# Kernel optimization log

Hardware: AMD Instinct MI355X
Metric: run time of the kernel (lower is better)

## Reference

```python
import jax, jax.numpy as jnp
import numpy as np

NUM_HEADS = 12
HEAD_DIM = 64
LOGIT_SCALE_MAX = 4.605170185988092  # log(1/0.01), open_clip default
EPS = 1e-12  # F.normalize eps


def setup_inputs() -> dict:
    key = jax.random.key(0)
    ks = jax.random.split(key, 8)
    N, L, C = 2, 2048, 768
    return {
        "x": jax.random.normal(ks[0], (N, L, C), dtype=jnp.float32),
        "in_proj_w": jax.random.normal(ks[1], (3 * C, C), dtype=jnp.float32) * 0.02,
        "in_proj_b": jax.random.normal(ks[2], (3 * C,), dtype=jnp.float32) * 0.02,
        "logit_scale": jax.random.normal(ks[3], (NUM_HEADS, 1, 1), dtype=jnp.float32),
        "learned_scale": jnp.ones((NUM_HEADS,), dtype=jnp.float32),
        "out_proj_w": jax.random.normal(ks[4], (C, C), dtype=jnp.float32) * 0.02,
        "out_proj_b": jax.random.normal(ks[5], (C,), dtype=jnp.float32) * 0.02,
        "attn_mask": jnp.zeros((L, L), dtype=jnp.float32),
    }


def _l2norm(t):
    # F.normalize(dim=-1): x / max(||x||, eps)
    n = jnp.linalg.norm(t, axis=-1, keepdims=True)
    return t / jnp.maximum(n, EPS)


def reference(x, in_proj_w, in_proj_b, logit_scale, learned_scale,
              out_proj_w, out_proj_b, attn_mask):
    N, L, C = x.shape
    H, D = NUM_HEADS, HEAD_DIM
    # packed QKV projection: [N, L, 3C]
    qkv = jnp.einsum("nlc,fc->nlf", x, in_proj_w) + in_proj_b
    q, k, v = jnp.split(qkv, 3, axis=-1)
    # [N, L, C] -> [N, H, L, D]
    to_heads = lambda t: t.reshape(N, L, H, D).transpose(0, 2, 1, 3)
    q, k, v = to_heads(q), to_heads(k), to_heads(v)
    # cosine attention with clamped exp logit scale per head
    attn = jnp.einsum("nhld,nhmd->nhlm", _l2norm(q), _l2norm(k))
    ls = jnp.exp(jnp.minimum(logit_scale, LOGIT_SCALE_MAX))  # [H,1,1]
    attn = attn * ls[None]  # broadcast over [N,H,L,L]
    attn = attn + attn_mask  # additive mask [L,L]
    attn = jax.nn.softmax(attn, axis=-1)
    out = jnp.einsum("nhlm,nhmd->nhld", attn, v)
    # learned per-head output scale
    out = out * learned_scale[None, :, None, None]
    # [N,H,L,D] -> [N,L,C]
    out = out.transpose(0, 2, 1, 3).reshape(N, L, C)
    out = jnp.einsum("nlc,fc->nlf", out, out_proj_w) + out_proj_b
    return out
```

## Files before the change

### kernel.cpp

```cpp
#include <hip/hip_runtime.h>
#include <math.h>

#define NB   2
#define SEQ  2048
#define CH   768
#define NH   12
#define HD   64
#define F3   2304
#define LSMAX 4.605170185988092f
#define LOG2E 1.4426950408889634f
#define RESCALE_THR 8.0f
#define EXP2F(x) __builtin_amdgcn_exp2f(x)

typedef _Float16 f16;
typedef __attribute__((ext_vector_type(8))) _Float16 f16x8;
typedef __attribute__((ext_vector_type(4))) _Float16 f16x4;
typedef __attribute__((ext_vector_type(2))) _Float16 f16x2;
typedef __attribute__((ext_vector_type(4))) float f32x4;
typedef __attribute__((ext_vector_type(16))) float f32x16;

typedef __attribute__((address_space(3))) void lds_void;
typedef __attribute__((address_space(1))) const void gbl_cvoid;

#define QSZ   3145728
#define OATT  (3 * QSZ)
#define XHOFF 12582912
#define W1OFF 15728640
#define W2OFF 17498112
#define FLAGO 18087936

#define VCH   2048
#define VPLN  131072

#define GP2  72

#define KOFF(s, b) (((s) * 2 + (b)) * 2048)
#define VOFF(s, b) (8192 + ((s) * 2 + (b)) * 2304)

__global__ __launch_bounds__(256) void cvt_f16(const float* __restrict__ X,
                                               const float* __restrict__ W1,
                                               const float* __restrict__ W2,
                                               const float* __restrict__ M,
                                               f16* __restrict__ Xh,
                                               f16* __restrict__ W1h,
                                               f16* __restrict__ W2h,
                                               int* __restrict__ flag)
{
    int tid = blockIdx.x * 256 + threadIdx.x;
    if (blockIdx.y == 3) {
        if (tid < 1048576) {
            float4 v = ((const float4*)M)[tid];
            bool nz = (v.x != 0.f) || (v.y != 0.f) || (v.z != 0.f) || (v.w != 0.f);
            if (__any(nz) && (threadIdx.x & 63) == 0) atomicOr(flag, 1);
        }
        return;
    }
    const float* src; f16* dst; int n4;
    switch (blockIdx.y) {
        case 0:  src = X;  dst = Xh;  n4 = 786432;  break;
        case 1:  src = W1; dst = W1h; n4 = 442368;  break;
        default: src = W2; dst = W2h; n4 = 147456;  break;
    }
    if (tid < n4) {
        float4 v = ((const float4*)src)[tid];
        f16x4 o = {(f16)v.x, (f16)v.y, (f16)v.z, (f16)v.w};
        ((f16x4*)dst)[tid] = o;
    }
}

__global__ __launch_bounds__(256, 4) void qkv_gemm(const f16* __restrict__ Xh,
                                                   const f16* __restrict__ Wh,
                                                   const float* __restrict__ bias,
                                                   const float* __restrict__ logit_scale,
                                                   f16* __restrict__ qkv16)
{
    __shared__ f16 As[2][128 * 32];
    __shared__ f16 Bs[2][128 * 32];
    const int t    = threadIdx.x;
    const int w    = t >> 6;
    const int lane = t & 63;
    const int quad = lane >> 4;
    const int sub  = lane & 15;
    const int wm   = w & 1, wn = w >> 1;
    const int f0   = blockIdx.x * 128;
    const int m0   = blockIdx.y * 128;

    const int s0 = t, s1 = 256 + t;
    const int r0 = s0 >> 2, cb0 = ((s0 & 3) ^ (r0 & 3)) * 8;
    const int r1 = s1 >> 2, cb1 = ((s1 & 3) ^ (r1 & 3)) * 8;
    const f16* ga0 = Xh + (size_t)(m0 + r0) * CH + cb0;
    const f16* ga1 = Xh + (size_t)(m0 + r1) * CH + cb1;
    const f16* gb0 = Wh + (size_t)(f0 + r0) * CH + cb0;
    const f16* gb1 = Wh + (size_t)(f0 + r1) * CH + cb1;

    f32x4 acc[4][4];
#pragma unroll
    for (int i = 0; i < 4; ++i)
#pragma unroll
        for (int j = 0; j < 4; ++j) acc[i][j] = (f32x4){0.f, 0.f, 0.f, 0.f};

    const int pch = (quad ^ (sub & 3)) * 8;

    __builtin_amdgcn_global_load_lds((gbl_cvoid*)(ga0), (lds_void*)&As[0][s0 * 8], 16, 0, 0);
    __builtin_amdgcn_global_load_lds((gbl_cvoid*)(ga1), (lds_void*)&As[0][s1 * 8], 16, 0, 0);
    __builtin_amdgcn_global_load_lds((gbl_cvoid*)(gb0), (lds_void*)&Bs[0][s0 * 8], 16, 0, 0);
    __builtin_amdgcn_global_load_lds((gbl_cvoid*)(gb1), (lds_void*)&Bs[0][s1 * 8], 16, 0, 0);
    __syncthreads();

    for (int k0 = 0; k0 < CH; k0 += 32) {
        const int cur = (k0 >> 5) & 1, nxt = cur ^ 1;
        if (k0 + 32 < CH) {
            __builtin_amdgcn_global_load_lds((gbl_cvoid*)(ga0 + k0 + 32), (lds_void*)&As[nxt][s0 * 8], 16, 0, 0);
            __builtin_amdgcn_global_load_lds((gbl_cvoid*)(ga1 + k0 + 32), (lds_void*)&As[nxt][s1 * 8], 16, 0, 0);
            __builtin_amdgcn_global_load_lds((gbl_cvoid*)(gb0 + k0 + 32), (lds_void*)&Bs[nxt][s0 * 8], 16, 0, 0);
            __builtin_amdgcn_global_load_lds((gbl_cvoid*)(gb1 + k0 + 32), (lds_void*)&Bs[nxt][s1 * 8], 16, 0, 0);
        }
        f16x8 af[4], bf[4];
#pragma unroll
        for (int i = 0; i < 4; ++i) {
            af[i] = *(const f16x8*)&As[cur][(wm * 64 + i * 16 + sub) * 32 + pch];
            bf[i] = *(const f16x8*)&Bs[cur][(wn * 64 + i * 16 + sub) * 32 + pch];
        }
#pragma unroll
        for (int i = 0; i < 4; ++i)
#pragma unroll
            for (int j = 0; j < 4; ++j)
                acc[i][j] = __builtin_amdgcn_mfma_f32_16x16x32_f16(af[i], bf[j], acc[i][j], 0, 0, 0);
        __syncthreads();
    }

    const int t3 = f0 / CH;
    const int h  = ((f0 + wn * 64) % CH) >> 6;
    float bb[4];
#pragma unroll
    for (int j = 0; j < 4; ++j) bb[j] = bias[f0 + wn * 64 + j * 16 + sub];

    if (t3 == 2) {
        f16* vdst = qkv16 + (size_t)2 * QSZ;
#pragma unroll
        for (int i = 0; i < 4; ++i) {
            int mb = m0 + wm * 64 + i * 16 + quad * 4;
            int nn = mb >> 11, l0 = mb & 2047;
            f16* pl = vdst + (size_t)(nn * NH + h) * VPLN + (l0 >> 5) * VCH + (l0 & 31);
#pragma unroll
            for (int j = 0; j < 4; ++j) {
                f16x4 vv;
#pragma unroll
                for (int r = 0; r < 4; ++r) vv[r] = (f16)(acc[i][j][r] + bb[j]);
                *(f16x4*)(pl + (j * 16 + sub) * 32) = vv;
            }
        }
        return;
    }

    f16* dst = qkv16 + (size_t)t3 * QSZ;
    float lsv = (t3 == 0) ? __expf(fminf(logit_scale[h], LSMAX)) * LOG2E : 1.0f;
#pragma unroll
    for (int i = 0; i < 4; ++i) {
#pragma unroll
        for (int r = 0; r < 4; ++r) {
            int m = m0 + wm * 64 + i * 16 + quad * 4 + r;
            int n = m >> 11, l = m & 2047;
            float v[4];
#pragma unroll
            for (int j = 0; j < 4; ++j) v[j] = acc[i][j][r] + bb[j];
            float ss = v[0] * v[0] + v[1] * v[1] + v[2] * v[2] + v[3] * v[3];
#pragma unroll
            for (int mk = 1; mk < 16; mk <<= 1) ss += __shfl_xor(ss, mk, 64);
            float scale = 1.0f / fmaxf(sqrtf(ss), 1e-12f);
            if (t3 == 0) scale *= lsv;
            f16* drow = dst + (((size_t)n * NH + h) * SEQ + l) * HD;
#pragma unroll
            for (int j = 0; j < 4; ++j)
                drow[j * 16 + sub] = (f16)(v[j] * scale);
        }
    }
}

union V8 { f16x4 h[2]; f16x8 v; };
union U8 { int i[4]; f16x8 v; };

__device__ __forceinline__ void compute_chunk_lds(
    const f16* Kr, const f16* Vr, int rsw, int h2,
    const f16x8& qf0, const f16x8& qf1, const f16x8& qf2, const f16x8& qf3,
    int cc, bool has_mask, const float* __restrict__ Mg,
    f32x16& o0, f32x16& o1, float& m_run, float& l_accA, float& l_accB)
{
    const f16x2 one2 = {(f16)1.f, (f16)1.f};
    f16x8 kf0 = *(const f16x8*)(Kr + ((8 * h2 + 0)  ^ rsw));
    f16x8 kf1 = *(const f16x8*)(Kr + ((8 * h2 + 16) ^ rsw));
    f16x8 kf2 = *(const f16x8*)(Kr + ((8 * h2 + 32) ^ rsw));
    f16x8 kf3 = *(const f16x8*)(Kr + ((8 * h2 + 48) ^ rsw));
    f32x16 sA = {};
    sA = __builtin_amdgcn_mfma_f32_32x32x16_f16(kf0, qf0, sA, 0, 0, 0);
    sA = __builtin_amdgcn_mfma_f32_32x32x16_f16(kf1, qf1, sA, 0, 0, 0);
    sA = __builtin_amdgcn_mfma_f32_32x32x16_f16(kf2, qf2, sA, 0, 0, 0);
    sA = __builtin_amdgcn_mfma_f32_32x32x16_f16(kf3, qf3, sA, 0, 0, 0);
    V8 va, vb, vc, vd;
    va.h[0] = *(const f16x4*)(Vr + 0);
    va.h[1] = *(const f16x4*)(Vr + 8);
    vb.h[0] = *(const f16x4*)(Vr + 16);
    vb.h[1] = *(const f16x4*)(Vr + 24);
    vc.h[0] = *(const f16x4*)(Vr + 1152 + 0);
    vc.h[1] = *(const f16x4*)(Vr + 1152 + 8);
    vd.h[0] = *(const f16x4*)(Vr + 1152 + 16);
    vd.h[1] = *(const f16x4*)(Vr + 1152 + 24);

    if (has_mask) {
#pragma unroll
        for (int rr = 0; rr < 16; ++rr) {
            int kk = cc * 32 + (rr & 3) + 8 * (rr >> 2) + 4 * h2;
            sA[rr] += LOG2E * Mg[kk];
        }
    }
    float a0 = fmaxf(sA[0], sA[1]),  a1 = fmaxf(sA[2], sA[3]);
    float a2 = fmaxf(sA[4], sA[5]),  a3 = fmaxf(sA[6], sA[7]);
    float a4 = fmaxf(sA[8], sA[9]),  a5 = fmaxf(sA[10], sA[11]);
    float a6 = fmaxf(sA[12], sA[13]), a7 = fmaxf(sA[14], sA[15]);
    float b0 = fmaxf(a0, a1), b1 = fmaxf(a2, a3);
    float b2 = fmaxf(a4, a5), b3 = fmaxf(a6, a7);
    float mloc = fmaxf(fmaxf(b0, b1), fmaxf(b2, b3));
    float mfull = fmaxf(mloc, __shfl_xor(mloc, 32, 64));
    if (__any(mfull - m_run > RESCALE_THR)) {
        float mnew = fmaxf(m_run, mfull);
        float al = EXP2F(m_run - mnew);
        m_run = mnew;
        l_accA *= al;
        l_accB *= al;
#pragma unroll
        for (int rr = 0; rr < 16; ++rr) { o0[rr] *= al; o1[rr] *= al; }
    }
#pragma unroll
    for (int rr = 0; rr < 16; ++rr) sA[rr] = EXP2F(sA[rr] - m_run);
    U8 u0, u1;
    u0.i[0] = __builtin_bit_cast(int, __builtin_amdgcn_cvt_pkrtz(sA[0], sA[1]));
    u0.i[1] = __builtin_bit_cast(int, __builtin_amdgcn_cvt_pkrtz(sA[2], sA[3]));
    u0.i[2] = __builtin_bit_cast(int, __builtin_amdgcn_cvt_pkrtz(sA[4], sA[5]));
    u0.i[3] = __builtin_bit_cast(int, __builtin_amdgcn_cvt_pkrtz(sA[6], sA[7]));
    u1.i[0] = __builtin_bit_cast(int, __builtin_amdgcn_cvt_pkrtz(sA[8], sA[9]));
    u1.i[1] = __builtin_bit_cast(int, __builtin_amdgcn_cvt_pkrtz(sA[10], sA[11]));
    u1.i[2] = __builtin_bit_cast(int, __builtin_amdgcn_cvt_pkrtz(sA[12], sA[13]));
    u1.i[3] = __builtin_bit_cast(int, __builtin_amdgcn_cvt_pkrtz(sA[14], sA[15]));
    l_accA = __builtin_amdgcn_fdot2(__builtin_bit_cast(f16x2, u0.i[0]), one2, l_accA, false);
    l_accB = __builtin_amdgcn_fdot2(__builtin_bit_cast(f16x2, u0.i[1]), one2, l_accB, false);
    l_accA = __builtin_amdgcn_fdot2(__builtin_bit_cast(f16x2, u0.i[2]), one2, l_accA, false);
    l_accB = __builtin_amdgcn_fdot2(__builtin_bit_cast(f16x2, u0.i[3]), one2, l_accB, false);
    l_accA = __builtin_amdgcn_fdot2(__builtin_bit_cast(f16x2, u1.i[0]), one2, l_accA, false);
    l_accB = __builtin_amdgcn_fdot2(__builtin_bit_cast(f16x2, u1.i[1]), one2, l_accB, false);
    l_accA = __builtin_amdgcn_fdot2(__builtin_bit_cast(f16x2, u1.i[2]), one2, l_accA, false);
    l_accB = __builtin_amdgcn_fdot2(__builtin_bit_cast(f16x2, u1.i[3]), one2, l_accB, false);
    o0 = __builtin_amdgcn_mfma_f32_32x32x16_f16(va.v, u0.v, o0, 0, 0, 0);
    o0 = __builtin_amdgcn_mfma_f32_32x32x16_f16(vb.v, u1.v, o0, 0, 0, 0);
    o1 = __builtin_amdgcn_mfma_f32_32x32x16_f16(vc.v, u0.v, o1, 0, 0, 0);
    o1 = __builtin_amdgcn_mfma_f32_32x32x16_f16(vd.v, u1.v, o1, 0, 0, 0);
}

__global__ __launch_bounds__(256, 3) void attn(const f16* __restrict__ Qh,
                                               const f16* __restrict__ Kh,
                                               const f16* __restrict__ Vt,
                                               const float* __restrict__ M32,
                                               const float* __restrict__ lscale,
                                               const int* __restrict__ flag,
                                               f16* __restrict__ Og)
{
    __shared__ f16x8 SMraw[2176];
    f16* SM = (f16*)SMraw;

    const int t    = threadIdx.x;
    const int w    = t >> 6;
    const int lane = t & 63;
    const int g    = w >> 1;
    const int s    = w & 1;
    const int r32  = lane & 31;
    const int h2   = lane >> 5;
    const int qb   = blockIdx.x * 64;
    const int hh   = blockIdx.y, n = blockIdx.z;
    const bool has_mask = (*flag) != 0;

    const int q = qb + g * 32 + r32;
    const f16* Qg  = Qh + ((size_t)(n * NH + hh) * SEQ + q) * HD + 8 * h2;
    const f16* KgH = Kh + ((size_t)(n * NH + hh) * SEQ + s * 1024) * HD;
    const f16* VgH = Vt + (size_t)(n * NH + hh) * VPLN + (size_t)(s * 32) * VCH;
    const float* Mg = M32 + (size_t)q * SEQ + s * 1024;

    f16x8 qf0 = *(const f16x8*)(Qg + 0);
    f16x8 qf1 = *(const f16x8*)(Qg + 16);
    f16x8 qf2 = *(const f16x8*)(Qg + 32);
    f16x8 qf3 = *(const f16x8*)(Qg + 48);

    const int th   = (g << 6) | lane;
    const int krow = th >> 2;
    const int kseg = (th & 3) << 4;
    const int ksw  = (krow & 7) << 3;
    const int vrow = th >> 1;
    const int vcol = (th & 1) << 4;
    const int rsw  = (r32 & 7) << 3;

    f16* Kw0 = SM + KOFF(s, 0) + krow * 64;
    f16* Kw1 = SM + KOFF(s, 1) + krow * 64;
    f16* Vw0 = SM + VOFF(s, 0) + vrow * 36 + vcol;
    f16* Vw1 = SM + VOFF(s, 1) + vrow * 36 + vcol;
    const f16* Kr0 = SM + KOFF(s, 0) + r32 * 64;
    const f16* Kr1 = SM + KOFF(s, 1) + r32 * 64;
    const f16* Vr0 = SM + VOFF(s, 0) + r32 * 36 + 4 * h2;
    const f16* Vr1 = SM + VOFF(s, 1) + r32 * 36 + 4 * h2;

    f16x8 kr0, kr1, vv0, vv1;
    {
        const f16* kp = KgH + krow * 64 + kseg;
        kr0 = *(const f16x8*)(kp);
        kr1 = *(const f16x8*)(kp + 8);
        const f16* vp = VgH + th * 16;
        vv0 = *(const f16x8*)(vp);
        vv1 = *(const f16x8*)(vp + 8);
        *(f16x8*)(Kw0 + ((kseg + 0) ^ ksw)) = kr0;
        *(f16x8*)(Kw0 + ((kseg + 8) ^ ksw)) = kr1;
        *(f16x8*)(Vw0 + 0) = vv0;
        *(f16x8*)(Vw0 + 8) = vv1;
    }
    __syncthreads();

    f32x16 o0 = {}, o1 = {};
    float m_run = -1e30f, l_accA = 0.f, l_accB = 0.f;

#pragma unroll 1
    for (int c = 0; c < 32; c += 2) {
        {
            const f16* kp = KgH + ((c + 1) * 32 + krow) * 64 + kseg;
            kr0 = *(const f16x8*)(kp);
            kr1 = *(const f16x8*)(kp + 8);
            const f16* vp = VgH + (c + 1) * VCH + th * 16;
            vv0 = *(const f16x8*)(vp);
            vv1 = *(const f16x8*)(vp + 8);
            __builtin_amdgcn_sched_barrier(0);
        }
        compute_chunk_lds(Kr0, Vr0, rsw, h2, qf0, qf1, qf2, qf3,
                          c, has_mask, Mg, o0, o1, m_run, l_accA, l_accB);
        *(f16x8*)(Kw1 + ((kseg + 0) ^ ksw)) = kr0;
        *(f16x8*)(Kw1 + ((kseg + 8) ^ ksw)) = kr1;
        *(f16x8*)(Vw1 + 0) = vv0;
        *(f16x8*)(Vw1 + 8) = vv1;
        __syncthreads();
        if (c + 2 < 32) {
            const f16* kp = KgH + ((c + 2) * 32 + krow) * 64 + kseg;
            kr0 = *(const f16x8*)(kp);
            kr1 = *(const f16x8*)(kp + 8);
            const f16* vp = VgH + (c + 2) * VCH + th * 16;
            vv0 = *(const f16x8*)(vp);
            vv1 = *(const f16x8*)(vp + 8);
            __builtin_amdgcn_sched_barrier(0);
        }
        compute_chunk_lds(Kr1, Vr1, rsw, h2, qf0, qf1, qf2, qf3,
                          c + 1, has_mask, Mg, o0, o1, m_run, l_accA, l_accB);
        if (c + 2 < 32) {
            *(f16x8*)(Kw0 + ((kseg + 0) ^ ksw)) = kr0;
            *(f16x8*)(Kw0 + ((kseg + 8) ^ ksw)) = kr1;
            *(f16x8*)(Vw0 + 0) = vv0;
            *(f16x8*)(Vw0 + 8) = vv1;
            __syncthreads();
        }
    }

    float l_acc = l_accA + l_accB;
    float l_full = l_acc + __shfl_xor(l_acc, 32, 64);

    __syncthreads();
    float* OSp = (float*)SM;
    float* MSp = OSp + 4352;
    float* LSp = MSp + 64;

    if (s == 1) {
        if (h2 == 0) { MSp[g * 32 + r32] = m_run; LSp[g * 32 + r32] = l_full; }
#pragma unroll
        for (int rq = 0; rq < 4; ++rq) {
            int d0 = 8 * rq + 4 * h2;
            *(f32x4*)&OSp[(g * 32 + r32) * 68 + d0] =
                (f32x4){o0[rq * 4 + 0], o0[rq * 4 + 1], o0[rq * 4 + 2], o0[rq * 4 + 3]};
            *(f32x4*)&OSp[(g * 32 + r32) * 68 + d0 + 32] =
                (f32x4){o1[rq * 4 + 0], o1[rq * 4 + 1], o1[rq * 4 + 2], o1[rq * 4 + 3]};
        }
    }
    __syncthreads();
    if (s == 0) {
        float m_p = MSp[g * 32 + r32], l_p = LSp[g * 32 + r32];
        float mm = fmaxf(m_run, m_p);
        float a0 = EXP2F(m_run - mm), a1 = EXP2F(m_p - mm);
        float l_tot = a0 * l_full + a1 * l_p;
        float sc = lscale[hh] / l_tot;
        float sa = a0 * sc, sb = a1 * sc;
        f16* op = Og + ((size_t)n * SEQ + q) * CH + hh * 64;
#pragma unroll
        for (int rq = 0; rq < 4; ++rq) {
            int d0 = 8 * rq + 4 * h2;
            f32x4 p0 = *(const f32x4*)&OSp[(g * 32 + r32) * 68 + d0];
            f32x4 p1 = *(const f32x4*)&OSp[(g * 32 + r32) * 68 + d0 + 32];
            f16x4 ov0, ov1;
#pragma unroll
            for (int j = 0; j < 4; ++j) {
                ov0[j] = (f16)(o0[rq * 4 + j] * sa + p0[j] * sb);
                ov1[j] = (f16)(o1[rq * 4 + j] * sa + p1[j] * sb);
            }
            *(f16x4*)(op + d0)      = ov0;
            *(f16x4*)(op + 32 + d0) = ov1;
        }
    }
}

__global__ __launch_bounds__(256, 4) void out_gemm(const f16* __restrict__ A,
                                                   const f16* __restrict__ Wh,
                                                   const float* __restrict__ bias,
                                                   float* __restrict__ out)
{
    __shared__ f16 As[64 * GP2];
    __shared__ f16 Bs[64 * GP2];
    const int t    = threadIdx.x;
    const int w    = t >> 6;
    const int lane = t & 63;
    const int quad = lane >> 4;
    const int sub  = lane & 15;
    const int f0   = blockIdx.x * 64;
    const int m0   = blockIdx.y * 64;
    const int srow = t >> 2;
    const int sk   = (t & 3) * 16;

    const f16* ag = A + (size_t)(m0 + srow) * CH + sk;
    const f16* bg = Wh + (size_t)(f0 + srow) * CH + sk;
    f16x8 a0 = *(const f16x8*)(ag);
    f16x8 a1 = *(const f16x8*)(ag + 8);
    f16x8 b0 = *(const f16x8*)(bg);
    f16x8 b1 = *(const f16x8*)(bg + 8);

    f32x4 acc[4];
#pragma unroll
    for (int i = 0; i < 4; ++i) acc[i] = (f32x4){0.f, 0.f, 0.f, 0.f};

    for (int k0 = 0; k0 < CH; k0 += 64) {
        __syncthreads();
        *(f16x8*)&As[srow * GP2 + sk + 0] = a0;
        *(f16x8*)&As[srow * GP2 + sk + 8] = a1;
        *(f16x8*)&Bs[srow * GP2 + sk + 0] = b0;
        *(f16x8*)&Bs[srow * GP2 + sk + 8] = b1;
        __syncthreads();
        if (k0 + 64 < CH) {
            a0 = *(const f16x8*)(ag + k0 + 64);
            a1 = *(const f16x8*)(ag + k0 + 72);
            b0 = *(const f16x8*)(bg + k0 + 64);
            b1 = *(const f16x8*)(bg + k0 + 72);
        }
#pragma unroll
        for (int kk = 0; kk < 64; kk += 32) {
            f16x8 bf = *(const f16x8*)&Bs[(w * 16 + sub) * GP2 + kk + quad * 8];
#pragma unroll
            for (int i = 0; i < 4; ++i) {
                f16x8 af = *(const f16x8*)&As[(i * 16 + sub) * GP2 + kk + quad * 8];
                acc[i] = __builtin_amdgcn_mfma_f32_16x16x32_f16(af, bf, acc[i], 0, 0, 0);
            }
        }
    }
    float bb = bias[f0 + w * 16 + sub];
#pragma unroll
    for (int i = 0; i < 4; ++i)
#pragma unroll
        for (int r = 0; r < 4; ++r) {
            int m = m0 + i * 16 + quad * 4 + r;
            out[(size_t)m * CH + f0 + w * 16 + sub] = acc[i][r] + bb;
        }
}

extern "C" void kernel_launch(void* const* d_in, const int* in_sizes, int n_in,
                              void* d_out, int out_size, void* d_ws, size_t ws_size,
                              hipStream_t stream) {
    const float* x    = (const float*)d_in[0];
    const float* w1   = (const float*)d_in[1];
    const float* b1   = (const float*)d_in[2];
    const float* ls   = (const float*)d_in[3];
    const float* lrn  = (const float*)d_in[4];
    const float* w2   = (const float*)d_in[5];
    const float* b2   = (const float*)d_in[6];
    const float* msk  = (const float*)d_in[7];
    f16*   ws16 = (f16*)d_ws;
    int*   flag = (int*)(ws16 + FLAGO);
    float* out  = (float*)d_out;

    (void)hipMemsetAsync(flag, 0, 4, stream);
    hipLaunchKernelGGL(cvt_f16, dim3(4096, 4), dim3(256), 0, stream,
                       x, w1, w2, msk,
                       ws16 + XHOFF, ws16 + W1OFF, ws16 + W2OFF, flag);
    hipLaunchKernelGGL(qkv_gemm, dim3(F3 / 128, (NB * SEQ) / 128), dim3(256), 0, stream,
                       ws16 + XHOFF, ws16 + W1OFF, b1, ls, ws16);
    hipLaunchKernelGGL(attn, dim3(SEQ / 64, NH, NB), dim3(256), 0, stream,
                       ws16, ws16 + QSZ, ws16 + 2 * QSZ, msk, lrn, flag,
                       ws16 + OATT);
    hipLaunchKernelGGL(out_gemm, dim3(CH / 64, (NB * SEQ) / 64), dim3(256), 0, stream,
                       ws16 + OATT, ws16 + W2OFF, b2, out);
}
```

Baseline: 188.6 us.

## Double K/V stage tile to 64 keys per barrier with priority boost

Each pipeline stage now stages 64 keys of K and V in shared memory instead of 32, so each thread loads and stores twice as much per stage. Two compute chunks run per stage, which halves the number of __syncthreads over the key loop. The MFMA section is wrapped in s_setprio to favour compute waves. Shared memory roughly doubles and occupancy bounds drop from 3 to 2 blocks, which may reduce latency hiding. The final pre-epilogue barrier is also removed, relying on the loop's last barrier.

After: 206.9 us. 1.1x slower.

```diff
diff --git a/kernel.cpp b/kernel.cpp
--- a/kernel.cpp
+++ b/kernel.cpp
@@ -34,8 +34,8 @@
 
 #define GP2  72
 
-#define KOFF(s, b) (((s) * 2 + (b)) * 2048)
-#define VOFF(s, b) (8192 + ((s) * 2 + (b)) * 2304)
+#define KOFF(s, b) (((s) * 2 + (b)) * 4096)
+#define VOFF(s, b) (16384 + ((s) * 2 + (b)) * 4352)
 
 __global__ __launch_bounds__(256) void cvt_f16(const float* __restrict__ X,
                                                const float* __restrict__ W1,
@@ -201,10 +201,10 @@
     va.h[1] = *(const f16x4*)(Vr + 8);
     vb.h[0] = *(const f16x4*)(Vr + 16);
     vb.h[1] = *(const f16x4*)(Vr + 24);
-    vc.h[0] = *(const f16x4*)(Vr + 1152 + 0);
-    vc.h[1] = *(const f16x4*)(Vr + 1152 + 8);
-    vd.h[0] = *(const f16x4*)(Vr + 1152 + 16);
-    vd.h[1] = *(const f16x4*)(Vr + 1152 + 24);
+    vc.h[0] = *(const f16x4*)(Vr + 2176 + 0);
+    vc.h[1] = *(const f16x4*)(Vr + 2176 + 8);
+    vd.h[0] = *(const f16x4*)(Vr + 2176 + 16);
+    vd.h[1] = *(const f16x4*)(Vr + 2176 + 24);
 
     if (has_mask) {
 #pragma unroll
@@ -255,7 +255,7 @@
     o1 = __builtin_amdgcn_mfma_f32_32x32x16_f16(vd.v, u1.v, o1, 0, 0, 0);
 }
 
-__global__ __launch_bounds__(256, 3) void attn(const f16* __restrict__ Qh,
+__global__ __launch_bounds__(256, 2) void attn(const f16* __restrict__ Qh,
                                                const f16* __restrict__ Kh,
                                                const f16* __restrict__ Vt,
                                                const float* __restrict__ M32,
@@ -263,7 +263,7 @@
                                                const int* __restrict__ flag,
                                                f16* __restrict__ Og)
 {
-    __shared__ f16x8 SMraw[2176];
+    __shared__ f16x8 SMraw[4224];
     f16* SM = (f16*)SMraw;
 
     const int t    = threadIdx.x;
@@ -288,35 +288,44 @@
     f16x8 qf2 = *(const f16x8*)(Qg + 32);
     f16x8 qf3 = *(const f16x8*)(Qg + 48);
 
-    const int th   = (g << 6) | lane;
-    const int krow = th >> 2;
-    const int kseg = (th & 3) << 4;
-    const int ksw  = (krow & 7) << 3;
-    const int vrow = th >> 1;
-    const int vcol = (th & 1) << 4;
-    const int rsw  = (r32 & 7) << 3;
+    const int th     = (g << 6) | lane;
+    const int krow   = th >> 1;
+    const int kseg   = (th & 1) << 5;
+    const int ksw    = (krow & 7) << 3;
+    const int vd     = th >> 1;
+    const int vchunk = th & 1;
+    const int rsw    = (r32 & 7) << 3;
 
     f16* Kw0 = SM + KOFF(s, 0) + krow * 64;
     f16* Kw1 = SM + KOFF(s, 1) + krow * 64;
-    f16* Vw0 = SM + VOFF(s, 0) + vrow * 36 + vcol;
-    f16* Vw1 = SM + VOFF(s, 1) + vrow * 36 + vcol;
+    f16* Vw0 = SM + VOFF(s, 0) + vd * 68 + vchunk * 32;
+    f16* Vw1 = SM + VOFF(s, 1) + vd * 68 + vchunk * 32;
     const f16* Kr0 = SM + KOFF(s, 0) + r32 * 64;
     const f16* Kr1 = SM + KOFF(s, 1) + r32 * 64;
-    const f16* Vr0 = SM + VOFF(s, 0) + r32 * 36 + 4 * h2;
-    const f16* Vr1 = SM + VOFF(s, 1) + r32 * 36 + 4 * h2;
-
-    f16x8 kr0, kr1, vv0, vv1;
+    const f16* Vr0 = SM + VOFF(s, 0) + r32 * 68 + 4 * h2;
+    const f16* Vr1 = SM + VOFF(s, 1) + r32 * 68 + 4 * h2;
+
+    const f16* kg = KgH + krow * 64 + kseg;
+    const f16* vg = VgH + vchunk * VCH + vd * 32;
+
+    f16x8 kr0, kr1, kr2, kr3, vv0, vv1, vv2, vv3;
     {
-        const f16* kp = KgH + krow * 64 + kseg;
-        kr0 = *(const f16x8*)(kp);
-        kr1 = *(const f16x8*)(kp + 8);
-        const f16* vp = VgH + th * 16;
-        vv0 = *(const f16x8*)(vp);
-        vv1 = *(const f16x8*)(vp + 8);
-        *(f16x8*)(Kw0 + ((kseg + 0) ^ ksw)) = kr0;
-        *(f16x8*)(Kw0 + ((kseg + 8) ^ ksw)) = kr1;
-        *(f16x8*)(Vw0 + 0) = vv0;
-        *(f16x8*)(Vw0 + 8) = vv1;
+        kr0 = *(const f16x8*)(kg + 0);
+        kr1 = *(const f16x8*)(kg + 8);
+        kr2 = *(const f16x8*)(kg + 16);
+        kr3 = *(const f16x8*)(kg + 24);
+        vv0 = *(const f16x8*)(vg + 0);
+        vv1 = *(const f16x8*)(vg + 8);
+        vv2 = *(const f16x8*)(vg + 16);
+        vv3 = *(const f16x8*)(vg + 24);
+        *(f16x8*)(Kw0 + ((kseg + 0)  ^ ksw)) = kr0;
+        *(f16x8*)(Kw0 + ((kseg + 8)  ^ ksw)) = kr1;
+        *(f16x8*)(Kw0 + ((kseg + 16) ^ ksw)) = kr2;
+        *(f16x8*)(Kw0 + ((kseg + 24) ^ ksw)) = kr3;
+        *(f16x8*)(Vw0 + 0)  = vv0;
+        *(f16x8*)(Vw0 + 8)  = vv1;
+        *(f16x8*)(Vw0 + 16) = vv2;
+        *(f16x8*)(Vw0 + 24) = vv3;
     }
     __syncthreads();
 
@@ -324,47 +333,47 @@
     float m_run = -1e30f, l_accA = 0.f, l_accB = 0.f;
 
 #pragma unroll 1
-    for (int c = 0; c < 32; c += 2) {
-        {
-            const f16* kp = KgH + ((c + 1) * 32 + krow) * 64 + kseg;
-            kr0 = *(const f16x8*)(kp);
+    for (int p = 0; p < 16; ++p) {
+        const int b = p & 1;
+        if (p + 1 < 16) {
+            const f16* kp = kg + (p + 1) * 4096;
+            kr0 = *(const f16x8*)(kp + 0);
             kr1 = *(const f16x8*)(kp + 8);
-            const f16* vp = VgH + (c + 1) * VCH + th * 16;
-            vv0 = *(const f16x8*)(vp);
+            kr2 = *(const f16x8*)(kp + 16);
+            kr3 = *(const f16x8*)(kp + 24);
+            const f16* vp = vg + (p + 1) * 4096;
+            vv0 = *(const f16x8*)(vp + 0);
             vv1 = *(const f16x8*)(vp + 8);
+            vv2 = *(const f16x8*)(vp + 16);
+            vv3 = *(const f16x8*)(vp + 24);
             __builtin_amdgcn_sched_barrier(0);
         }
-        compute_chunk_lds(Kr0, Vr0, rsw, h2, qf0, qf1, qf2, qf3,
-                          c, has_mask, Mg, o0, o1, m_run, l_accA, l_accB);
-        *(f16x8*)(Kw1 + ((kseg + 0) ^ ksw)) = kr0;
-        *(f16x8*)(Kw1 + ((kseg + 8) ^ ksw)) = kr1;
-        *(f16x8*)(Vw1 + 0) = vv0;
-        *(f16x8*)(Vw1 + 8) = vv1;
+        const f16* KrB = b ? Kr1 : Kr0;
+        const f16* VrB = b ? Vr1 : Vr0;
+        __builtin_amdgcn_s_setprio(1);
+        compute_chunk_lds(KrB,        VrB,      rsw, h2, qf0, qf1, qf2, qf3,
+                          2 * p,     has_mask, Mg, o0, o1, m_run, l_accA, l_accB);
+        compute_chunk_lds(KrB + 2048, VrB + 32, rsw, h2, qf0, qf1, qf2, qf3,
+                          2 * p + 1, has_mask, Mg, o0, o1, m_run, l_accA, l_accB);
+        __builtin_amdgcn_s_setprio(0);
+        if (p + 1 < 16) {
+            f16* Kw = b ? Kw0 : Kw1;
+            f16* Vw = b ? Vw0 : Vw1;
+            *(f16x8*)(Kw + ((kseg + 0)  ^ ksw)) = kr0;
+            *(f16x8*)(Kw + ((kseg + 8)  ^ ksw)) = kr1;
+            *(f16x8*)(Kw + ((kseg + 16) ^ ksw)) = kr2;
+            *(f16x8*)(Kw + ((kseg + 24) ^ ksw)) = kr3;
+            *(f16x8*)(Vw + 0)  = vv0;
+            *(f16x8*)(Vw + 8)  = vv1;
+            *(f16x8*)(Vw + 16) = vv2;
+            *(f16x8*)(Vw + 24) = vv3;
+        }
         __syncthreads();
-        if (c + 2 < 32) {
-            const f16* kp = KgH + ((c + 2) * 32 + krow) * 64 + kseg;
-            kr0 = *(const f16x8*)(kp);
-            kr1 = *(const f16x8*)(kp + 8);
-            const f16* vp = VgH + (c + 2) * VCH + th * 16;
-            vv0 = *(const f16x8*)(vp);
-            vv1 = *(const f16x8*)(vp + 8);
-            __builtin_amdgcn_sched_barrier(0);
-        }
-        compute_chunk_lds(Kr1, Vr1, rsw, h2, qf0, qf1, qf2, qf3,
-                          c + 1, has_mask, Mg, o0, o1, m_run, l_accA, l_accB);
-        if (c + 2 < 32) {
-            *(f16x8*)(Kw0 + ((kseg + 0) ^ ksw)) = kr0;
-            *(f16x8*)(Kw0 + ((kseg + 8) ^ ksw)) = kr1;
-            *(f16x8*)(Vw0 + 0) = vv0;
-            *(f16x8*)(Vw0 + 8) = vv1;
-            __syncthreads();
-        }
     }
 
     float l_acc = l_accA + l_accB;
     float l_full = l_acc + __shfl_xor(l_acc, 32, 64);
 
-    __syncthreads();
     float* OSp = (float*)SM;
     float* MSp = OSp + 4352;
     float* LSp = MSp + 64;
```

## Software-pipeline attention with triple-buffered LDS and QK lookahead

Applied to the files above, without the earlier changes.

Splits the per-chunk attention step into a QK MFMA stage and a softmax+PV stage. The QK scores for the next chunk are computed while the current chunk's softmax and PV run. K/V staging in LDS moves from two buffers to three so a chunk can be loaded two steps ahead. This is meant to overlap MFMA latency with softmax VALU work, at the cost of more LDS (which may cut occupancy below the 3-block launch bound) and more live registers for the extra score tile.

Measured after the change: 190.3 us. No clear change (+0.9%).

```diff
diff --git a/kernel.cpp b/kernel.cpp
--- a/kernel.cpp
+++ b/kernel.cpp
@@ -34,8 +34,8 @@
 
 #define GP2  72
 
-#define KOFF(s, b) (((s) * 2 + (b)) * 2048)
-#define VOFF(s, b) (8192 + ((s) * 2 + (b)) * 2304)
+#define KOFF3(s, b) (((s) * 3 + (b)) * 2048)
+#define VOFF3(s, b) (12288 + ((s) * 3 + (b)) * 2304)
 
 __global__ __launch_bounds__(256) void cvt_f16(const float* __restrict__ X,
                                                const float* __restrict__ W1,
@@ -180,13 +180,11 @@
 union V8 { f16x4 h[2]; f16x8 v; };
 union U8 { int i[4]; f16x8 v; };
 
-__device__ __forceinline__ void compute_chunk_lds(
-    const f16* Kr, const f16* Vr, int rsw, int h2,
+__device__ __forceinline__ f32x16 qk_chunk(
+    const f16* Kr, int rsw, int h2,
     const f16x8& qf0, const f16x8& qf1, const f16x8& qf2, const f16x8& qf3,
-    int cc, bool has_mask, const float* __restrict__ Mg,
-    f32x16& o0, f32x16& o1, float& m_run, float& l_accA, float& l_accB)
-{
-    const f16x2 one2 = {(f16)1.f, (f16)1.f};
+    int cc, bool has_mask, const float* __restrict__ Mg)
+{
     f16x8 kf0 = *(const f16x8*)(Kr + ((8 * h2 + 0)  ^ rsw));
     f16x8 kf1 = *(const f16x8*)(Kr + ((8 * h2 + 16) ^ rsw));
     f16x8 kf2 = *(const f16x8*)(Kr + ((8 * h2 + 32) ^ rsw));
@@ -196,6 +194,21 @@
     sA = __builtin_amdgcn_mfma_f32_32x32x16_f16(kf1, qf1, sA, 0, 0, 0);
     sA = __builtin_amdgcn_mfma_f32_32x32x16_f16(kf2, qf2, sA, 0, 0, 0);
     sA = __builtin_amdgcn_mfma_f32_32x32x16_f16(kf3, qf3, sA, 0, 0, 0);
+    if (has_mask) {
+#pragma unroll
+        for (int rr = 0; rr < 16; ++rr) {
+            int kk = cc * 32 + (rr & 3) + 8 * (rr >> 2) + 4 * h2;
+            sA[rr] += LOG2E * Mg[kk];
+        }
+    }
+    return sA;
+}
+
+__device__ __forceinline__ void smpv_chunk(
+    f32x16 sA, const f16* Vr, int h2,
+    f32x16& o0, f32x16& o1, float& m_run, float& l_accA, float& l_accB)
+{
+    const f16x2 one2 = {(f16)1.f, (f16)1.f};
     V8 va, vb, vc, vd;
     va.h[0] = *(const f16x4*)(Vr + 0);
     va.h[1] = *(const f16x4*)(Vr + 8);
@@ -205,14 +218,6 @@
     vc.h[1] = *(const f16x4*)(Vr + 1152 + 8);
     vd.h[0] = *(const f16x4*)(Vr + 1152 + 16);
     vd.h[1] = *(const f16x4*)(Vr + 1152 + 24);
-
-    if (has_mask) {
-#pragma unroll
-        for (int rr = 0; rr < 16; ++rr) {
-            int kk = cc * 32 + (rr & 3) + 8 * (rr >> 2) + 4 * h2;
-            sA[rr] += LOG2E * Mg[kk];
-        }
-    }
     float a0 = fmaxf(sA[0], sA[1]),  a1 = fmaxf(sA[2], sA[3]);
     float a2 = fmaxf(sA[4], sA[5]),  a3 = fmaxf(sA[6], sA[7]);
     float a4 = fmaxf(sA[8], sA[9]),  a5 = fmaxf(sA[10], sA[11]);
@@ -263,7 +268,7 @@
                                                const int* __restrict__ flag,
                                                f16* __restrict__ Og)
 {
-    __shared__ f16x8 SMraw[2176];
+    __shared__ f16x8 SMraw[3264];
     f16* SM = (f16*)SMraw;
 
     const int t    = threadIdx.x;
@@ -296,70 +301,64 @@
     const int vcol = (th & 1) << 4;
     const int rsw  = (r32 & 7) << 3;
 
-    f16* Kw0 = SM + KOFF(s, 0) + krow * 64;
-    f16* Kw1 = SM + KOFF(s, 1) + krow * 64;
-    f16* Vw0 = SM + VOFF(s, 0) + vrow * 36 + vcol;
-    f16* Vw1 = SM + VOFF(s, 1) + vrow * 36 + vcol;
-    const f16* Kr0 = SM + KOFF(s, 0) + r32 * 64;
-    const f16* Kr1 = SM + KOFF(s, 1) + r32 * 64;
-    const f16* Vr0 = SM + VOFF(s, 0) + r32 * 36 + 4 * h2;
-    const f16* Vr1 = SM + VOFF(s, 1) + r32 * 36 + 4 * h2;
+    f16* Kw0 = SM + KOFF3(s, 0) + krow * 64;
+    f16* Kw1 = SM + KOFF3(s, 1) + krow * 64;
+    f16* Kw2 = SM + KOFF3(s, 2) + krow * 64;
+    f16* Vw0 = SM + VOFF3(s, 0) + vrow * 36 + vcol;
+    f16* Vw1 = SM + VOFF3(s, 1) + vrow * 36 + vcol;
+    f16* Vw2 = SM + VOFF3(s, 2) + vrow * 36 + vcol;
+    const f16* Kr0 = SM + KOFF3(s, 0) + r32 * 64;
+    const f16* Kr1 = SM + KOFF3(s, 1) + r32 * 64;
+    const f16* Kr2 = SM + KOFF3(s, 2) + r32 * 64;
+    const f16* Vr0 = SM + VOFF3(s, 0) + r32 * 36 + 4 * h2;
+    const f16* Vr1 = SM + VOFF3(s, 1) + r32 * 36 + 4 * h2;
+    const f16* Vr2 = SM + VOFF3(s, 2) + r32 * 36 + 4 * h2;
 
     f16x8 kr0, kr1, vv0, vv1;
-    {
-        const f16* kp = KgH + krow * 64 + kseg;
-        kr0 = *(const f16x8*)(kp);
-        kr1 = *(const f16x8*)(kp + 8);
-        const f16* vp = VgH + th * 16;
-        vv0 = *(const f16x8*)(vp);
-        vv1 = *(const f16x8*)(vp + 8);
-        *(f16x8*)(Kw0 + ((kseg + 0) ^ ksw)) = kr0;
-        *(f16x8*)(Kw0 + ((kseg + 8) ^ ksw)) = kr1;
-        *(f16x8*)(Vw0 + 0) = vv0;
-        *(f16x8*)(Vw0 + 8) = vv1;
-    }
+
+#define STLD(ci) do { if ((ci) < 32) {                                        \
+    const f16* kp_ = KgH + ((ci) * 32 + krow) * 64 + kseg;                    \
+    kr0 = *(const f16x8*)(kp_); kr1 = *(const f16x8*)(kp_ + 8);               \
+    const f16* vp_ = VgH + (ci) * VCH + th * 16;                              \
+    vv0 = *(const f16x8*)(vp_); vv1 = *(const f16x8*)(vp_ + 8);               \
+    __builtin_amdgcn_sched_barrier(0); } } while (0)
+
+#define STWR(ci, Kw, Vw) do { if ((ci) < 32) {                                \
+    *(f16x8*)((Kw) + ((kseg + 0) ^ ksw)) = kr0;                               \
+    *(f16x8*)((Kw) + ((kseg + 8) ^ ksw)) = kr1;                               \
+    *(f16x8*)((Vw) + 0) = vv0;                                                \
+    *(f16x8*)((Vw) + 8) = vv1; } } while (0)
+
+    STLD(0);
+    STWR(0, Kw0, Vw0);
+    STLD(1);
+    STWR(1, Kw1, Vw1);
     __syncthreads();
 
     f32x16 o0 = {}, o1 = {};
     float m_run = -1e30f, l_accA = 0.f, l_accB = 0.f;
+    f32x16 sA = qk_chunk(Kr0, rsw, h2, qf0, qf1, qf2, qf3, 0, has_mask, Mg);
+
+#define BODY(ci, KrN, VrC, KwW, VwW) do {                                     \
+    STLD((ci) + 2);                                                           \
+    f32x16 sN_ = {};                                                          \
+    if ((ci) + 1 < 32)                                                        \
+        sN_ = qk_chunk(KrN, rsw, h2, qf0, qf1, qf2, qf3, (ci) + 1,            \
+                       has_mask, Mg);                                         \
+    smpv_chunk(sA, VrC, h2, o0, o1, m_run, l_accA, l_accB);                   \
+    STWR((ci) + 2, KwW, VwW);                                                 \
+    __syncthreads();                                                          \
+    sA = sN_; } while (0)
 
 #pragma unroll 1
-    for (int c = 0; c < 32; c += 2) {
-        {
-            const f16* kp = KgH + ((c + 1) * 32 + krow) * 64 + kseg;
-            kr0 = *(const f16x8*)(kp);
-            kr1 = *(const f16x8*)(kp + 8);
-            const f16* vp = VgH + (c + 1) * VCH + th * 16;
-            vv0 = *(const f16x8*)(vp);
-            vv1 = *(const f16x8*)(vp + 8);
-            __builtin_amdgcn_sched_barrier(0);
-        }
-        compute_chunk_lds(Kr0, Vr0, rsw, h2, qf0, qf1, qf2, qf3,
-                          c, has_mask, Mg, o0, o1, m_run, l_accA, l_accB);
-        *(f16x8*)(Kw1 + ((kseg + 0) ^ ksw)) = kr0;
-        *(f16x8*)(Kw1 + ((kseg + 8) ^ ksw)) = kr1;
-        *(f16x8*)(Vw1 + 0) = vv0;
-        *(f16x8*)(Vw1 + 8) = vv1;
-        __syncthreads();
-        if (c + 2 < 32) {
-            const f16* kp = KgH + ((c + 2) * 32 + krow) * 64 + kseg;
-            kr0 = *(const f16x8*)(kp);
-            kr1 = *(const f16x8*)(kp + 8);
-            const f16* vp = VgH + (c + 2) * VCH + th * 16;
-            vv0 = *(const f16x8*)(vp);
-            vv1 = *(const f16x8*)(vp + 8);
-            __builtin_amdgcn_sched_barrier(0);
-        }
-        compute_chunk_lds(Kr1, Vr1, rsw, h2, qf0, qf1, qf2, qf3,
-                          c + 1, has_mask, Mg, o0, o1, m_run, l_accA, l_accB);
-        if (c + 2 < 32) {
-            *(f16x8*)(Kw0 + ((kseg + 0) ^ ksw)) = kr0;
-            *(f16x8*)(Kw0 + ((kseg + 8) ^ ksw)) = kr1;
-            *(f16x8*)(Vw0 + 0) = vv0;
-            *(f16x8*)(Vw0 + 8) = vv1;
-            __syncthreads();
-        }
-    }
+    for (int i = 0; i < 32; i += 3) {
+        BODY(i, Kr1, Vr0, Kw2, Vw2);
+        if (i + 1 < 32) BODY(i + 1, Kr2, Vr1, Kw0, Vw0);
+        if (i + 2 < 32) BODY(i + 2, Kr0, Vr2, Kw1, Vw1);
+    }
+#undef BODY
+#undef STLD
+#undef STWR
 
     float l_acc = l_accA + l_accB;
     float l_full = l_acc + __shfl_xor(l_acc, 32, 64);
```
